# Kernel tuning notes

Hardware: AMD Instinct MI355X
Metric: run time of the kernel (lower is better)

Reference implementation:

```python
import jax, jax.numpy as jnp
import numpy as np

TAU = [1, 2, 4, 8]
B, T, FC, FX = 128, 2048, 512, 512


def setup_inputs() -> dict:
    key = jax.random.key(0)
    k1, k2, k3, k4 = jax.random.split(key, 4)
    C = jax.random.normal(k1, (B, T, FC), dtype=jnp.float32)
    X = jax.random.normal(k2, (B, T, FX), dtype=jnp.float32)
    # one Linear(encoding_size -> context_size) per tau; torch weight layout [out, in]
    W = jax.random.normal(k3, (len(TAU), FC, FX), dtype=jnp.float32) * (1.0 / np.sqrt(FX))
    b = jax.random.normal(k4, (len(TAU), FC), dtype=jnp.float32) * 0.01
    return {"C": C, "X": X, "W": W, "b": b}


def _infonce(Ct, Xe, Wk, bk):
    # Ct: [B, Tt, fc], Xe: [B, Tt, fx]
    Xt = jnp.einsum('btf,gf->btg', Xe, Wk) + bk          # Linear: [B, Tt, fc]
    Z = jnp.einsum('itf,jtf->ijt', Ct, Xt)               # scores [B, B, Tt]
    Zmax = jnp.max(Z, axis=1, keepdims=True)             # [B, 1, Tt]
    lse = jnp.log(jnp.sum(jnp.exp(Z - Zmax), axis=1)) + Zmax[:, 0]  # [B, Tt]
    Zdiag = jnp.diagonal(Z, axis1=0, axis2=1).T          # Z[i,i,t] -> [B, Tt]
    return jnp.mean(Zdiag - lse)


def reference(C, X, W, b):
    losses = [_infonce(C[:, :-t], X[:, t:], W[k], b[k]) for k, t in enumerate(TAU)]
    return jnp.stack(losses)
```

## Files before the change

### kernel.cpp

```cpp
#include <hip/hip_runtime.h>
#include <math.h>

constexpr int Tn  = 2048;
constexpr int FCn = 512;
constexpr int FXn = 512;
constexpr int SXW = 72;
constexpr int SYC = 136;
constexpr int SZS = 132;

typedef __attribute__((ext_vector_type(8))) short  bf16x8;
typedef __attribute__((ext_vector_type(4))) float  f32x4;

__device__ __forceinline__ unsigned pk2(float a, float b) {
  return __builtin_amdgcn_perm(__float_as_uint(b), __float_as_uint(a), 0x07060302u);
}
__device__ __forceinline__ uint4 pack8(float4 a, float4 b) {
  uint4 rv;
  rv.x = pk2(a.x, a.y); rv.y = pk2(a.z, a.w);
  rv.z = pk2(b.x, b.y); rv.w = pk2(b.z, b.w);
  return rv;
}

__global__ void zero4(float* out) {
  if (threadIdx.x < 4) out[threadIdx.x] = 0.0f;
}

__global__ void finalize4(float* out) {
  int k = threadIdx.x;
  if (k < 4) out[k] *= 1.0f / (128.0f * (float)(Tn - (1 << k)));
}

__global__ void wconv(const float* __restrict__ W, unsigned short* __restrict__ Wh) {
  int i = blockIdx.x * 256 + threadIdx.x;
  float4 v = *((const float4*)W + i);
  uint2 p; p.x = pk2(v.x, v.y); p.y = pk2(v.z, v.w);
  *((uint2*)Wh + i) = p;
}

template <bool WBF>
__global__ __launch_bounds__(512, 4)
void infonce_main(const float* __restrict__ Cp, const float* __restrict__ Xp,
                  const void* __restrict__ Wp, float* __restrict__ out)
{
  __shared__ __align__(16) unsigned char smem[71680];
  unsigned short* sX = (unsigned short*)(smem);
  unsigned short* sW = (unsigned short*)(smem + 18432);
  unsigned short* sY = (unsigned short*)(smem + 36864);
  unsigned short* sC = (unsigned short*)(smem);
  float* sZ   = (float*)(smem);
  float* sRed = (float*)(smem + 67584);

  const int tid  = threadIdx.x;
  const int lane = tid & 63;
  const int wave = tid >> 6;
  const int r    = lane & 15;
  const int h    = lane >> 4;
  const int wr   = wave >> 1;
  const int wc   = wave & 1;

  const int orig = blockIdx.x;
  const int xcd  = orig & 7;
  const int loc  = orig >> 3;
  const int wg   = (xcd < 4) ? (xcd * 1024 + loc) : (4096 + (xcd - 4) * 1023 + loc);
  const int k    = wg & 3;
  const int t    = wg >> 2;
  const int tau  = 1 << k;
  if (t >= Tn - tau) return;

  const float* Cb = Cp + (size_t)t * FCn;
  const float* Xb = Xp + (size_t)(t + tau) * FXn;

  const int srow = tid >> 2;
  const int scol = (tid & 3) * 16;
  const float* xs = Xb + (size_t)srow * (Tn * FXn) + scol;
  unsigned short* xd = sX + srow * SXW + scol;
  unsigned short* wd = sW + srow * SXW + scol;
  const unsigned short* wsh = (const unsigned short*)Wp + (size_t)k * (FCn * FXn)
                              + (size_t)srow * FXn + scol;
  const float* wsf = (const float*)Wp + (size_t)k * (FCn * FXn)
                     + (size_t)srow * FXn + scol;
  const int crow0 = tid >> 4;
  const int ccol  = (tid & 15) * 8;
  const float* cs = Cb + (size_t)crow0 * (Tn * FCn) + ccol;
  unsigned short* cd = sC + crow0 * SYC + ccol;
  const size_t cstep = (size_t)32 * Tn * FCn;

  float4 px0, px1, px2, px3;
  float4 pw0, pw1, pw2, pw3;
  uint4  pb0, pb1;
  float4 pc0, pc1, pc2, pc3, pc4, pc5, pc6, pc7;

#define LOAD_X(XC) do { \
    const float4* _p = (const float4*)(xs + (XC) * 64); \
    px0 = _p[0]; px1 = _p[1]; px2 = _p[2]; px3 = _p[3]; } while (0)
#define LOAD_W(GC, XC) do { \
    if constexpr (WBF) { \
      const uint4* _p = (const uint4*)(wsh + (size_t)((GC) * 128) * FXn + (XC) * 64); \
      pb0 = _p[0]; pb1 = _p[1]; \
    } else { \
      const float4* _p = (const float4*)(wsf + (size_t)((GC) * 128) * FXn + (XC) * 64); \
      pw0 = _p[0]; pw1 = _p[1]; pw2 = _p[2]; pw3 = _p[3]; } } while (0)
#define STORE_XW() do { \
    *(uint4*)(xd)     = pack8(px0, px1); \
    *(uint4*)(xd + 8) = pack8(px2, px3); \
    if constexpr (WBF) { *(uint4*)(wd) = pb0; *(uint4*)(wd + 8) = pb1; } \
    else { *(uint4*)(wd) = pack8(pw0, pw1); *(uint4*)(wd + 8) = pack8(pw2, pw3); } \
  } while (0)
#define MFMA_Y() do { \
    _Pragma("unroll") \
    for (int ks = 0; ks < 2; ++ks) { \
      const int xoo = ks * 32 + h * 8; \
      bf16x8 a0 = *(const bf16x8*)(sX + (wr * 32 + 0  + r) * SXW + xoo); \
      bf16x8 a1 = *(const bf16x8*)(sX + (wr * 32 + 16 + r) * SXW + xoo); \
      _Pragma("unroll") \
      for (int bg = 0; bg < 4; ++bg) { \
        bf16x8 bb = *(const bf16x8*)(sW + (wc * 64 + bg * 16 + r) * SXW + xoo); \
        yacc[0][bg] = __builtin_amdgcn_mfma_f32_16x16x32_bf16(a0, bb, yacc[0][bg], 0, 0, 0); \
        yacc[1][bg] = __builtin_amdgcn_mfma_f32_16x16x32_bf16(a1, bb, yacc[1][bg], 0, 0, 0); \
      } } } while (0)

  f32x4 zacc[2][4];
#pragma unroll
  for (int a = 0; a < 2; ++a)
#pragma unroll
    for (int b = 0; b < 4; ++b) zacc[a][b] = f32x4{0.f, 0.f, 0.f, 0.f};

  LOAD_X(0); LOAD_W(0, 0);

  for (int gc = 0; gc < 4; ++gc) {
    f32x4 yacc[2][4];
#pragma unroll
    for (int a = 0; a < 2; ++a)
#pragma unroll
      for (int b = 0; b < 4; ++b) yacc[a][b] = f32x4{0.f, 0.f, 0.f, 0.f};

    for (int xc = 0; xc < 7; ++xc) {
      __syncthreads();
      STORE_XW();
      __syncthreads();
      LOAD_X(xc + 1); LOAD_W(gc, xc + 1);
      MFMA_Y();
    }
    __syncthreads();
    STORE_XW();
    __syncthreads();
    {
      const float4* p0 = (const float4*)(cs + 0 * cstep + gc * 128);
      const float4* p1 = (const float4*)(cs + 1 * cstep + gc * 128);
      const float4* p2 = (const float4*)(cs + 2 * cstep + gc * 128);
      const float4* p3 = (const float4*)(cs + 3 * cstep + gc * 128);
      pc0 = p0[0]; pc1 = p0[1];
      pc2 = p1[0]; pc3 = p1[1];
      pc4 = p2[0]; pc5 = p2[1];
      pc6 = p3[0]; pc7 = p3[1];
    }
    MFMA_Y();

#pragma unroll
    for (int aj = 0; aj < 2; ++aj)
#pragma unroll
      for (int bg = 0; bg < 4; ++bg)
#pragma unroll
        for (int reg = 0; reg < 4; ++reg)
          sY[(wr * 32 + aj * 16 + h * 4 + reg) * SYC + (wc * 64 + bg * 16 + r)] =
              (unsigned short)(__float_as_uint(yacc[aj][bg][reg]) >> 16);
    __syncthreads();
    *(uint4*)(cd + 0 * 32 * SYC) = pack8(pc0, pc1);
    *(uint4*)(cd + 1 * 32 * SYC) = pack8(pc2, pc3);
    *(uint4*)(cd + 2 * 32 * SYC) = pack8(pc4, pc5);
    *(uint4*)(cd + 3 * 32 * SYC) = pack8(pc6, pc7);
    __syncthreads();
    if (gc < 3) { LOAD_X(0); LOAD_W(gc + 1, 0); }
#pragma unroll
    for (int ks = 0; ks < 4; ++ks) {
      const int go = ks * 32 + h * 8;
      bf16x8 a0 = *(const bf16x8*)(sC + (wr * 32 + 0  + r) * SYC + go);
      bf16x8 a1 = *(const bf16x8*)(sC + (wr * 32 + 16 + r) * SYC + go);
#pragma unroll
      for (int bj = 0; bj < 4; ++bj) {
        bf16x8 bb = *(const bf16x8*)(sY + (wc * 64 + bj * 16 + r) * SYC + go);
        zacc[0][bj] = __builtin_amdgcn_mfma_f32_16x16x32_bf16(a0, bb, zacc[0][bj], 0, 0, 0);
        zacc[1][bj] = __builtin_amdgcn_mfma_f32_16x16x32_bf16(a1, bb, zacc[1][bj], 0, 0, 0);
      }
    }
  }
  __syncthreads();
#pragma unroll
  for (int ai = 0; ai < 2; ++ai)
#pragma unroll
    for (int bj = 0; bj < 4; ++bj)
#pragma unroll
      for (int reg = 0; reg < 4; ++reg)
        sZ[(wr * 32 + ai * 16 + h * 4 + reg) * SZS + (wc * 64 + bj * 16 + r)] =
            zacc[ai][bj][reg];
  __syncthreads();

  const int row = wave * 16 + (lane >> 2);
  const int c0l = lane & 3;
  float mx = -3.4e38f;
#pragma unroll
  for (int m = 0; m < 32; ++m) mx = fmaxf(mx, sZ[row * SZS + c0l + m * 4]);
  mx = fmaxf(mx, __shfl_xor(mx, 1));
  mx = fmaxf(mx, __shfl_xor(mx, 2));
  float sum = 0.f;
#pragma unroll
  for (int m = 0; m < 32; ++m) sum += __expf(sZ[row * SZS + c0l + m * 4] - mx);
  sum += __shfl_xor(sum, 1);
  sum += __shfl_xor(sum, 2);
  float val = (c0l == 0) ? (sZ[row * SZS + row] - (__logf(sum) + mx)) : 0.f;
#pragma unroll
  for (int off = 1; off < 64; off <<= 1) val += __shfl_xor(val, off);
  if (lane == 0) sRed[wave] = val;
  __syncthreads();
  if (tid == 0) {
    float bs = 0.f;
#pragma unroll
    for (int w2 = 0; w2 < 8; ++w2) bs += sRed[w2];
    atomicAdd(out + k, bs);
  }
#undef LOAD_X
#undef LOAD_W
#undef STORE_XW
#undef MFMA_Y
}

extern "C" void kernel_launch(void* const* d_in, const int* in_sizes, int n_in,
                              void* d_out, int out_size, void* d_ws, size_t ws_size,
                              hipStream_t stream) {
  const float* C = (const float*)d_in[0];
  const float* X = (const float*)d_in[1];
  const float* W = (const float*)d_in[2];
  float* out = (float*)d_out;

  hipLaunchKernelGGL(zero4, dim3(1), dim3(64), 0, stream, out);
  const size_t wbytes = (size_t)4 * FCn * FXn * 2;
  if (ws_size >= wbytes) {
    hipLaunchKernelGGL(wconv, dim3(1024), dim3(256), 0, stream,
                       W, (unsigned short*)d_ws);
    hipLaunchKernelGGL(infonce_main<true>, dim3(2047 * 4), dim3(512), 0, stream,
                       C, X, (const void*)d_ws, out);
  } else {
    hipLaunchKernelGGL(infonce_main<false>, dim3(2047 * 4), dim3(512), 0, stream,
                       C, X, (const void*)W, out);
  }
  hipLaunchKernelGGL(finalize4, dim3(1), dim3(64), 0, stream, out);
}
```

Baseline: 1.483 ms.

## Pre-convert X and C to bf16 in workspace and load C fragments directly

Adds conversion passes that write X (and C when the workspace is large enough) to bf16 in workspace, plus a new main kernel that reads bf16 operands. This halves the bytes each block streams for X and C, which are re-read across the four tau values. The new kernel also loads C fragments straight from global memory into MFMA registers instead of staging them through shared memory, and folds the next-chunk prefetch into the inner loop. The cost is the extra conversion passes over 128 MB inputs, and whether this path runs depends on workspace size.

```diff
diff --git a/kernel.cpp b/kernel.cpp
--- a/kernel.cpp
+++ b/kernel.cpp
@@ -30,11 +30,181 @@
   if (k < 4) out[k] *= 1.0f / (128.0f * (float)(Tn - (1 << k)));
 }
 
-__global__ void wconv(const float* __restrict__ W, unsigned short* __restrict__ Wh) {
+__global__ void tobf16(const float* __restrict__ s, unsigned short* __restrict__ d) {
   int i = blockIdx.x * 256 + threadIdx.x;
-  float4 v = *((const float4*)W + i);
+  float4 v = ((const float4*)s)[i];
   uint2 p; p.x = pk2(v.x, v.y); p.y = pk2(v.z, v.w);
-  *((uint2*)Wh + i) = p;
+  ((uint2*)d)[i] = p;
+}
+
+template <bool CBF>
+__global__ __launch_bounds__(512, 4)
+void infonce_bf16(const void* __restrict__ Cany, const unsigned short* __restrict__ Xb,
+                  const unsigned short* __restrict__ Wb, float* __restrict__ out)
+{
+  __shared__ __align__(16) unsigned char smem[71680];
+  unsigned short* sX = (unsigned short*)(smem);
+  unsigned short* sW = (unsigned short*)(smem + 18432);
+  unsigned short* sY = (unsigned short*)(smem + 36864);
+  float* sZ   = (float*)(smem);
+  float* sRed = (float*)(smem + 67584);
+
+  const int tid  = threadIdx.x;
+  const int lane = tid & 63;
+  const int wave = tid >> 6;
+  const int r    = lane & 15;
+  const int h    = lane >> 4;
+  const int wr   = wave >> 1;
+  const int wc   = wave & 1;
+
+  const int orig = blockIdx.x;
+  const int xcd  = orig & 7;
+  const int loc  = orig >> 3;
+  const int wg   = (xcd < 4) ? (xcd * 1024 + loc) : (4096 + (xcd - 4) * 1023 + loc);
+  const int k    = wg & 3;
+  const int t    = wg >> 2;
+  const int tau  = 1 << k;
+  if (t >= Tn - tau) return;
+
+  const int srow = tid >> 2;
+  const int scol = (tid & 3) * 16;
+  const unsigned short* xs = Xb + (size_t)srow * (Tn * FXn)
+                             + (size_t)(t + tau) * FXn + scol;
+  const unsigned short* ws = Wb + (size_t)k * (FCn * FXn) + (size_t)srow * FXn + scol;
+  unsigned short* xd = sX + srow * SXW + scol;
+  unsigned short* wd = sW + srow * SXW + scol;
+
+  const unsigned short* c0h = nullptr; const unsigned short* c1h = nullptr;
+  const float*          c0f = nullptr; const float*          c1f = nullptr;
+  if constexpr (CBF) {
+    c0h = (const unsigned short*)Cany + (size_t)(wr * 32 + r) * (Tn * FCn)
+          + (size_t)t * FCn;
+    c1h = c0h + (size_t)16 * (Tn * FCn);
+  } else {
+    c0f = (const float*)Cany + (size_t)(wr * 32 + r) * (Tn * FCn) + (size_t)t * FCn;
+    c1f = c0f + (size_t)16 * (Tn * FCn);
+  }
+
+  uint4 px0, px1, pw0, pw1;
+
+#define LOAD_X(XC) do { \
+    const uint4* _p = (const uint4*)(xs + (XC) * 64); \
+    px0 = _p[0]; px1 = _p[1]; } while (0)
+#define LOAD_W(GC, XC) do { \
+    const uint4* _p = (const uint4*)(ws + (size_t)((GC) * 128) * FXn + (XC) * 64); \
+    pw0 = _p[0]; pw1 = _p[1]; } while (0)
+#define STORE_XW() do { \
+    *(uint4*)(xd) = px0; *(uint4*)(xd + 8) = px1; \
+    *(uint4*)(wd) = pw0; *(uint4*)(wd + 8) = pw1; } while (0)
+#define MFMA_Y() do { \
+    _Pragma("unroll") \
+    for (int ks = 0; ks < 2; ++ks) { \
+      const int xoo = ks * 32 + h * 8; \
+      bf16x8 a0 = *(const bf16x8*)(sX + (wr * 32 + 0  + r) * SXW + xoo); \
+      bf16x8 a1 = *(const bf16x8*)(sX + (wr * 32 + 16 + r) * SXW + xoo); \
+      _Pragma("unroll") \
+      for (int bg = 0; bg < 4; ++bg) { \
+        bf16x8 bb = *(const bf16x8*)(sW + (wc * 64 + bg * 16 + r) * SXW + xoo); \
+        yacc[0][bg] = __builtin_amdgcn_mfma_f32_16x16x32_bf16(a0, bb, yacc[0][bg], 0, 0, 0); \
+        yacc[1][bg] = __builtin_amdgcn_mfma_f32_16x16x32_bf16(a1, bb, yacc[1][bg], 0, 0, 0); \
+      } } } while (0)
+
+  f32x4 zacc[2][4];
+#pragma unroll
+  for (int a = 0; a < 2; ++a)
+#pragma unroll
+    for (int b = 0; b < 4; ++b) zacc[a][b] = f32x4{0.f, 0.f, 0.f, 0.f};
+
+  LOAD_X(0); LOAD_W(0, 0);
+
+  for (int gc = 0; gc < 4; ++gc) {
+    f32x4 yacc[2][4];
+#pragma unroll
+    for (int a = 0; a < 2; ++a)
+#pragma unroll
+      for (int b = 0; b < 4; ++b) yacc[a][b] = f32x4{0.f, 0.f, 0.f, 0.f};
+
+#pragma unroll 1
+    for (int xc = 0; xc < 8; ++xc) {
+      __syncthreads();
+      STORE_XW();
+      __syncthreads();
+      if (xc < 7)      { LOAD_X(xc + 1); LOAD_W(gc, xc + 1); }
+      else if (gc < 3) { LOAD_X(0);      LOAD_W(gc + 1, 0); }
+      MFMA_Y();
+    }
+
+#pragma unroll
+    for (int aj = 0; aj < 2; ++aj)
+#pragma unroll
+      for (int bg = 0; bg < 4; ++bg)
+#pragma unroll
+        for (int reg = 0; reg < 4; ++reg)
+          sY[(wr * 32 + aj * 16 + h * 4 + reg) * SYC + (wc * 64 + bg * 16 + r)] =
+              (unsigned short)(__float_as_uint(yacc[aj][bg][reg]) >> 16);
+    __syncthreads();
+
+#pragma unroll
+    for (int ks = 0; ks < 4; ++ks) {
+      const int go = ks * 32 + h * 8;
+      bf16x8 a0, a1;
+      if constexpr (CBF) {
+        a0 = *(const bf16x8*)(c0h + gc * 128 + go);
+        a1 = *(const bf16x8*)(c1h + gc * 128 + go);
+      } else {
+        float4 ca = *(const float4*)(c0f + gc * 128 + go);
+        float4 cb = *(const float4*)(c0f + gc * 128 + go + 4);
+        float4 cc = *(const float4*)(c1f + gc * 128 + go);
+        float4 cd = *(const float4*)(c1f + gc * 128 + go + 4);
+        a0 = __builtin_bit_cast(bf16x8, pack8(ca, cb));
+        a1 = __builtin_bit_cast(bf16x8, pack8(cc, cd));
+      }
+#pragma unroll
+      for (int bj = 0; bj < 4; ++bj) {
+        bf16x8 bb = *(const bf16x8*)(sY + (wc * 64 + bj * 16 + r) * SYC + go);
+        zacc[0][bj] = __builtin_amdgcn_mfma_f32_16x16x32_bf16(a0, bb, zacc[0][bj], 0, 0, 0);
+        zacc[1][bj] = __builtin_amdgcn_mfma_f32_16x16x32_bf16(a1, bb, zacc[1][bj], 0, 0, 0);
+      }
+    }
+  }
+  __syncthreads();
+#pragma unroll
+  for (int ai = 0; ai < 2; ++ai)
+#pragma unroll
+    for (int bj = 0; bj < 4; ++bj)
+#pragma unroll
+      for (int reg = 0; reg < 4; ++reg)
+        sZ[(wr * 32 + ai * 16 + h * 4 + reg) * SZS + (wc * 64 + bj * 16 + r)] =
+            zacc[ai][bj][reg];
+  __syncthreads();
+
+  const int row = wave * 16 + (lane >> 2);
+  const int c0l = lane & 3;
+  float mx = -3.4e38f;
+#pragma unroll
+  for (int m = 0; m < 32; ++m) mx = fmaxf(mx, sZ[row * SZS + c0l + m * 4]);
+  mx = fmaxf(mx, __shfl_xor(mx, 1));
+  mx = fmaxf(mx, __shfl_xor(mx, 2));
+  float sum = 0.f;
+#pragma unroll
+  for (int m = 0; m < 32; ++m) sum += __expf(sZ[row * SZS + c0l + m * 4] - mx);
+  sum += __shfl_xor(sum, 1);
+  sum += __shfl_xor(sum, 2);
+  float val = (c0l == 0) ? (sZ[row * SZS + row] - (__logf(sum) + mx)) : 0.f;
+#pragma unroll
+  for (int off = 1; off < 64; off <<= 1) val += __shfl_xor(val, off);
+  if (lane == 0) sRed[wave] = val;
+  __syncthreads();
+  if (tid == 0) {
+    float bs = 0.f;
+#pragma unroll
+    for (int w2 = 0; w2 < 8; ++w2) bs += sRed[w2];
+    atomicAdd(out + k, bs);
+  }
+#undef LOAD_X
+#undef LOAD_W
+#undef STORE_XW
+#undef MFMA_Y
 }
 
 template <bool WBF>
@@ -232,10 +402,30 @@
   const float* W = (const float*)d_in[2];
   float* out = (float*)d_out;
 
+  const size_t NX = (size_t)128 * Tn * FXn;
+  const size_t NW = (size_t)4 * FCn * FXn;
+  const size_t WS_W    = NW * 2;
+  const size_t WS_MID  = WS_W + NX * 2;
+  const size_t WS_FULL = WS_MID + NX * 2;
+
   hipLaunchKernelGGL(zero4, dim3(1), dim3(64), 0, stream, out);
-  const size_t wbytes = (size_t)4 * FCn * FXn * 2;
-  if (ws_size >= wbytes) {
-    hipLaunchKernelGGL(wconv, dim3(1024), dim3(256), 0, stream,
+
+  if (ws_size >= WS_MID) {
+    unsigned short* Wbf = (unsigned short*)d_ws;
+    unsigned short* Xbf = (unsigned short*)((char*)d_ws + WS_W);
+    hipLaunchKernelGGL(tobf16, dim3((unsigned)(NW / 1024)), dim3(256), 0, stream, W, Wbf);
+    hipLaunchKernelGGL(tobf16, dim3((unsigned)(NX / 1024)), dim3(256), 0, stream, X, Xbf);
+    if (ws_size >= WS_FULL) {
+      unsigned short* Cbf = (unsigned short*)((char*)d_ws + WS_MID);
+      hipLaunchKernelGGL(tobf16, dim3((unsigned)(NX / 1024)), dim3(256), 0, stream, C, Cbf);
+      hipLaunchKernelGGL(infonce_bf16<true>, dim3(2047 * 4), dim3(512), 0, stream,
+                         (const void*)Cbf, Xbf, Wbf, out);
+    } else {
+      hipLaunchKernelGGL(infonce_bf16<false>, dim3(2047 * 4), dim3(512), 0, stream,
+                         (const void*)C, Xbf, Wbf, out);
+    }
+  } else if (ws_size >= WS_W) {
+    hipLaunchKernelGGL(tobf16, dim3((unsigned)(NW / 1024)), dim3(256), 0, stream,
                        W, (unsigned short*)d_ws);
     hipLaunchKernelGGL(infonce_main<true>, dim3(2047 * 4), dim3(512), 0, stream,
                        C, X, (const void*)d_ws, out);
```

Result: no change. 1.455 ms (-1.9%).

## Add pre-converted bf16 X path with direct-to-LDS loads and larger per-wave tiles

Applied to the files above, without the earlier changes.

Adds a pass that converts all of X to bf16 in workspace, and a new main kernel that uses 256 threads. The kernel fills LDS with global_load_lds DMA into an XOR-swizzled layout and computes larger register tiles (64x128 Y per wave over 256-wide g chunks). C is read straight from global into registers, with no LDS staging. This is meant to halve X read traffic in the hot kernel, cut VGPR staging and LDS bank conflicts, and raise MFMA work per LDS read. The costs are an extra full-X conversion pass (read fp32, write bf16), higher register pressure from 128 accumulator vectors, and dependence on a large workspace, with a fallback to the old path when it is missing.

```diff
diff --git a/kernel.cpp b/kernel.cpp
--- a/kernel.cpp
+++ b/kernel.cpp
@@ -21,6 +21,12 @@
   return rv;
 }
 
+__device__ __forceinline__ void gll16(const unsigned short* g, void* lds) {
+  __builtin_amdgcn_global_load_lds(
+      (const __attribute__((address_space(1))) unsigned int*)g,
+      (__attribute__((address_space(3))) unsigned int*)lds, 16, 0, 0);
+}
+
 __global__ void zero4(float* out) {
   if (threadIdx.x < 4) out[threadIdx.x] = 0.0f;
 }
@@ -30,11 +36,168 @@
   if (k < 4) out[k] *= 1.0f / (128.0f * (float)(Tn - (1 << k)));
 }
 
-__global__ void wconv(const float* __restrict__ W, unsigned short* __restrict__ Wh) {
+__global__ void tobf16(const float* __restrict__ s, unsigned short* __restrict__ d) {
   int i = blockIdx.x * 256 + threadIdx.x;
-  float4 v = *((const float4*)W + i);
+  float4 v = ((const float4*)s)[i];
   uint2 p; p.x = pk2(v.x, v.y); p.y = pk2(v.z, v.w);
-  *((uint2*)Wh + i) = p;
+  ((uint2*)d)[i] = p;
+}
+
+__global__ __launch_bounds__(256, 2)
+void infonce_v7(const float* __restrict__ Cp, const unsigned short* __restrict__ Xb,
+                const unsigned short* __restrict__ Wb, float* __restrict__ out)
+{
+  __shared__ __align__(16) unsigned char smem[67648];
+  char* sm   = (char*)smem;
+  char* sWc  = sm + 16384;
+  float* sZ  = (float*)sm;
+  float* sRed = (float*)(sm + 67584);
+
+  const int tid  = threadIdx.x;
+  const int lane = tid & 63;
+  const int wave = tid >> 6;
+  const int r    = lane & 15;
+  const int h    = lane >> 4;
+  const int jw   = wave >> 1;
+  const int gw   = wave & 1;
+  const int iw   = wave >> 1;
+  const int jw2  = wave & 1;
+
+  const int orig = blockIdx.x;
+  const int xcd  = orig & 7;
+  const int loc  = orig >> 3;
+  const int wg   = (xcd < 4) ? (xcd * 1024 + loc) : (4096 + (xcd - 4) * 1023 + loc);
+  const int k    = wg & 3;
+  const int t    = wg >> 2;
+  const int tau  = 1 << k;
+  if (t >= Tn - tau) return;
+  const int s = t + tau;
+
+  const int colg = (lane & 7) ^ (lane >> 3);
+  const unsigned short* xlane = Xb + (size_t)(wave * 32 + (lane >> 3)) * (Tn * FXn)
+                                + (size_t)s * FXn + colg * 8;
+  const unsigned short* wlane = Wb + (size_t)k * (FCn * FXn)
+                                + (size_t)(wave * 64 + (lane >> 3)) * FXn + colg * 8;
+  char* xdst = sm  + wave * 4096;
+  char* wdst = sWc + wave * 8192;
+
+  const float* cr0 = Cp + (size_t)(iw * 64 +  0 + r) * (Tn * FCn) + (size_t)t * FCn;
+  const float* cr1 = Cp + (size_t)(iw * 64 + 16 + r) * (Tn * FCn) + (size_t)t * FCn;
+  const float* cr2 = Cp + (size_t)(iw * 64 + 32 + r) * (Tn * FCn) + (size_t)t * FCn;
+  const float* cr3 = Cp + (size_t)(iw * 64 + 48 + r) * (Tn * FCn) + (size_t)t * FCn;
+
+  f32x4 zacc[4][4];
+#pragma unroll
+  for (int a = 0; a < 4; ++a)
+#pragma unroll
+    for (int b = 0; b < 4; ++b) zacc[a][b] = f32x4{0.f, 0.f, 0.f, 0.f};
+
+#pragma unroll 1
+  for (int gc = 0; gc < 2; ++gc) {
+    f32x4 yacc[4][8];
+#pragma unroll
+    for (int a = 0; a < 4; ++a)
+#pragma unroll
+      for (int b = 0; b < 8; ++b) yacc[a][b] = f32x4{0.f, 0.f, 0.f, 0.f};
+
+#pragma unroll 1
+    for (int xc = 0; xc < 8; ++xc) {
+      __syncthreads();
+#pragma unroll
+      for (int i = 0; i < 4; ++i)
+        gll16(xlane + (size_t)(i * 8) * (Tn * FXn) + xc * 64, xdst + i * 1024);
+#pragma unroll
+      for (int i = 0; i < 8; ++i)
+        gll16(wlane + (size_t)(gc * 256 + i * 8) * FXn + xc * 64, wdst + i * 1024);
+      __syncthreads();
+#pragma unroll
+      for (int ks = 0; ks < 2; ++ks) {
+        const int cbx = (ks * 64 + h * 16) ^ ((r & 7) << 4);
+        bf16x8 ax[4], bw[8];
+#pragma unroll
+        for (int bm = 0; bm < 4; ++bm)
+          ax[bm] = *(const bf16x8*)(sm + (jw * 64 + bm * 16 + r) * 128 + cbx);
+#pragma unroll
+        for (int bn = 0; bn < 8; ++bn)
+          bw[bn] = *(const bf16x8*)(sWc + (gw * 128 + bn * 16 + r) * 128 + cbx);
+#pragma unroll
+        for (int bm = 0; bm < 4; ++bm)
+#pragma unroll
+          for (int bn = 0; bn < 8; ++bn)
+            yacc[bm][bn] = __builtin_amdgcn_mfma_f32_16x16x32_bf16(
+                ax[bm], bw[bn], yacc[bm][bn], 0, 0, 0);
+      }
+    }
+    __syncthreads();
+#pragma unroll
+    for (int bm = 0; bm < 4; ++bm)
+#pragma unroll
+      for (int bn = 0; bn < 8; ++bn)
+#pragma unroll
+        for (int reg = 0; reg < 4; ++reg) {
+          const int row = jw * 64 + bm * 16 + h * 4 + reg;
+          const int col = gw * 128 + bn * 16 + r;
+          *(unsigned short*)(sm + row * 528 + col * 2) =
+              (unsigned short)(__float_as_uint(yacc[bm][bn][reg]) >> 16);
+        }
+    __syncthreads();
+#pragma unroll 2
+    for (int ks2 = 0; ks2 < 8; ++ks2) {
+      const int goff = gc * 256 + ks2 * 32 + h * 8;
+      const int gb   = ks2 * 64 + h * 16;
+      bf16x8 ac[4], by[4];
+      {
+        float4 u0 = *(const float4*)(cr0 + goff);
+        float4 v0 = *(const float4*)(cr0 + goff + 4);
+        float4 u1 = *(const float4*)(cr1 + goff);
+        float4 v1 = *(const float4*)(cr1 + goff + 4);
+        float4 u2 = *(const float4*)(cr2 + goff);
+        float4 v2 = *(const float4*)(cr2 + goff + 4);
+        float4 u3 = *(const float4*)(cr3 + goff);
+        float4 v3 = *(const float4*)(cr3 + goff + 4);
+        ac[0] = __builtin_bit_cast(bf16x8, pack8(u0, v0));
+        ac[1] = __builtin_bit_cast(bf16x8, pack8(u1, v1));
+        ac[2] = __builtin_bit_cast(bf16x8, pack8(u2, v2));
+        ac[3] = __builtin_bit_cast(bf16x8, pack8(u3, v3));
+      }
+#pragma unroll
+      for (int bn = 0; bn < 4; ++bn)
+        by[bn] = *(const bf16x8*)(sm + (jw2 * 64 + bn * 16 + r) * 528 + gb);
+#pragma unroll
+      for (int bm = 0; bm < 4; ++bm)
+#pragma unroll
+        for (int bn = 0; bn < 4; ++bn)
+          zacc[bm][bn] = __builtin_amdgcn_mfma_f32_16x16x32_bf16(
+              ac[bm], by[bn], zacc[bm][bn], 0, 0, 0);
+    }
+  }
+  __syncthreads();
+#pragma unroll
+  for (int bm = 0; bm < 4; ++bm)
+#pragma unroll
+    for (int bn = 0; bn < 4; ++bn)
+#pragma unroll
+      for (int reg = 0; reg < 4; ++reg)
+        sZ[(iw * 64 + bm * 16 + h * 4 + reg) * SZS + (jw2 * 64 + bn * 16 + r)] =
+            zacc[bm][bn][reg];
+  __syncthreads();
+
+  const int row = wave * 32 + (lane >> 1);
+  const int c0l = lane & 1;
+  float mx = -3.4e38f;
+#pragma unroll
+  for (int m = 0; m < 64; ++m) mx = fmaxf(mx, sZ[row * SZS + c0l + m * 2]);
+  mx = fmaxf(mx, __shfl_xor(mx, 1));
+  float sum = 0.f;
+#pragma unroll
+  for (int m = 0; m < 64; ++m) sum += __expf(sZ[row * SZS + c0l + m * 2] - mx);
+  sum += __shfl_xor(sum, 1);
+  float val = (c0l == 0) ? (sZ[row * SZS + row] - (__logf(sum) + mx)) : 0.f;
+#pragma unroll
+  for (int off = 1; off < 64; off <<= 1) val += __shfl_xor(val, off);
+  if (lane == 0) sRed[wave] = val;
+  __syncthreads();
+  if (tid == 0) atomicAdd(out + k, sRed[0] + sRed[1] + sRed[2] + sRed[3]);
 }
 
 template <bool WBF>
@@ -232,10 +395,22 @@
   const float* W = (const float*)d_in[2];
   float* out = (float*)d_out;
 
+  const size_t NX = (size_t)128 * Tn * FXn;
+  const size_t NW = (size_t)4 * FCn * FXn;
+  const size_t WS_W   = NW * 2;
+  const size_t WS_MID = WS_W + NX * 2;
+
   hipLaunchKernelGGL(zero4, dim3(1), dim3(64), 0, stream, out);
-  const size_t wbytes = (size_t)4 * FCn * FXn * 2;
-  if (ws_size >= wbytes) {
-    hipLaunchKernelGGL(wconv, dim3(1024), dim3(256), 0, stream,
+
+  if (ws_size >= WS_MID) {
+    unsigned short* Wbf = (unsigned short*)d_ws;
+    unsigned short* Xbf = (unsigned short*)((char*)d_ws + WS_W);
+    hipLaunchKernelGGL(tobf16, dim3((unsigned)(NW / 1024)), dim3(256), 0, stream, W, Wbf);
+    hipLaunchKernelGGL(tobf16, dim3((unsigned)(NX / 1024)), dim3(256), 0, stream, X, Xbf);
+    hipLaunchKernelGGL(infonce_v7, dim3(2047 * 4), dim3(256), 0, stream,
+                       C, Xbf, Wbf, out);
+  } else if (ws_size >= WS_W) {
+    hipLaunchKernelGGL(tobf16, dim3((unsigned)(NW / 1024)), dim3(256), 0, stream,
                        W, (unsigned short*)d_ws);
     hipLaunchKernelGGL(infonce_main<true>, dim3(2047 * 4), dim3(512), 0, stream,
                        C, X, (const void*)d_ws, out);
```

New measurement: 1.364 ms. 1.09x faster.
